# Performance work log

Measured on AMD Instinct MI355X. Metric: run time of the kernel, lower is better.

Reference implementation:

```python
import jax, jax.numpy as jnp
import numpy as np

B, S, N, D, H = 128, 512, 32, 512, 2  # batch, seq_len, num_size, node_dim, hop_size
NPAD = 4  # padded number slots per row


def _lin(key, fi, fo):
    return 0.02 * jax.random.normal(key, (H, fi, fo), jnp.float32), jnp.zeros((H, fo), jnp.float32)


def setup_inputs() -> dict:
    key = jax.random.key(0)
    ks = jax.random.split(key, 12)
    encoder_outputs = jax.random.normal(ks[0], (S, B, D), jnp.float32)
    num_encoder_outputs = jax.random.normal(ks[1], (B, N, D), jnp.float32)
    # distinct positions per row in [0, S), last NPAD slots padded with -1
    num_pos_pad = jnp.argsort(jax.random.uniform(ks[2], (B, S)), axis=-1)[:, :N].astype(jnp.int32)
    num_pos_pad = num_pos_pad.at[:, -NPAD:].set(-1)
    # order ranks 1..N (random permutation per row), 0 on padded slots
    num_order_pad = (jnp.argsort(jax.random.uniform(ks[3], (B, N)), axis=-1) + 1).astype(jnp.int32)
    num_order_pad = num_order_pad.at[:, -NPAD:].set(0)
    w_n1a, b_n1a = _lin(ks[4], D, D)
    w_n1b, b_n1b = _lin(ks[5], D, D)
    w_n2a, b_n2a = _lin(ks[6], D, D)
    w_n2b, b_n2b = _lin(ks[7], D, D)
    w_g, b_g = _lin(ks[8], 4 * D, D)
    w_o, b_o = _lin(ks[9], 2 * D, D)
    return dict(encoder_outputs=encoder_outputs, num_encoder_outputs=num_encoder_outputs,
                num_pos_pad=num_pos_pad, num_order_pad=num_order_pad,
                w_n1a=w_n1a, b_n1a=b_n1a, w_n1b=w_n1b, b_n1b=b_n1b,
                w_n2a=w_n2a, b_n2a=b_n2a, w_n2b=w_n2b, b_n2b=b_n2b,
                w_g=w_g, b_g=b_g, w_o=w_o, b_o=b_o)


def reference(encoder_outputs, num_encoder_outputs, num_pos_pad, num_order_pad,
              w_n1a, b_n1a, w_n1b, b_n1b, w_n2a, b_n2a, w_n2b, b_n2b,
              w_g, b_g, w_o, b_o):
    node_mask = (num_order_pad > 0)                              # [B,N]
    greater = num_order_pad[:, :, None] > num_order_pad[:, None, :]
    lower = ~greater                                             # <=
    eye = jnp.eye(N, dtype=jnp.float32)
    pair = (node_mask[:, None, :] & node_mask[:, :, None]).astype(jnp.float32) * (1.0 - eye)
    g_gt = pair * greater.astype(jnp.float32) + eye              # [B,N,N]
    g_lt = pair * lower.astype(jnp.float32) + eye
    # row-normalize (D^{-1} A); diagonal guarantees row sums >= 1
    g_gt = g_gt / g_gt.sum(-1, keepdims=True)
    g_lt = g_lt / g_lt.sum(-1, keepdims=True)

    node = num_encoder_outputs                                   # [B,N,D]
    for h in range(H):
        ni1 = jax.nn.relu(jnp.einsum('bnm,bmd,de->bne', g_gt, node, w_n1a[h]) + b_n1a[h])
        ni1 = jax.nn.relu(jnp.einsum('bnm,bmd,de->bne', g_gt, ni1, w_n1b[h]) + b_n1b[h])
        ni2 = jax.nn.relu(jnp.einsum('bnm,bmd,de->bne', g_lt, node, w_n2a[h]) + b_n2a[h])
        ni2 = jax.nn.relu(jnp.einsum('bnm,bmd,de->bne', g_lt, ni2, w_n2b[h]) + b_n2b[h])
        gate_in = jnp.concatenate([ni1, ni2, ni1 + ni2, ni1 - ni2], axis=-1)
        gate = jax.nn.sigmoid(gate_in @ w_g[h] + b_g[h])
        node_info = gate * ni1 + (1.0 - gate) * ni2
        node = jax.nn.relu(jnp.concatenate([node, node_info], axis=-1) @ w_o[h] + b_o[h])

    # scatter node embeddings into padded [B, S+1, D]; pads -> slot S (dropped)
    num_mask = num_pos_pad > -1
    clamped = jnp.where(num_mask, num_pos_pad, S)                # [B,N]
    gnn_info = jnp.zeros((B, S + 1, D), jnp.float32)
    gnn_info = gnn_info.at[jnp.arange(B)[:, None], clamped].set(node)
    gnn_info = gnn_info[:, :S, :].transpose(1, 0, 2)             # [S,B,D]
    gnn_info = encoder_outputs + gnn_info
    num_embedding = num_encoder_outputs + node
    problem_output = jnp.max(gnn_info, axis=0)                   # [B,D]
    return gnn_info, num_embedding, problem_output
```

## Files before the change

### kernel.cpp

```cpp
#include <hip/hip_runtime.h>
#include <math.h>

#define BB 128
#define SS 512
#define NN 32
#define DD 512
#define HH 2
#define MM (BB * NN)
#define DSQ (DD * DD)

typedef short bf16x8 __attribute__((ext_vector_type(8)));
typedef float f32x4 __attribute__((ext_vector_type(4)));

__device__ __forceinline__ unsigned short f2bf(float f) {
    unsigned int u = __float_as_uint(f);
    u += 0x7fffu + ((u >> 16) & 1u);
    return (unsigned short)(u >> 16);
}
__device__ __forceinline__ float bf2f(unsigned short h) {
    return __uint_as_float(((unsigned int)h) << 16);
}
__device__ __forceinline__ void g2l16(const void* gp, void* lp) {
    __builtin_amdgcn_global_load_lds(
        (const __attribute__((address_space(1))) void*)gp,
        (__attribute__((address_space(3))) void*)lp, 16, 0, 0);
}

__global__ __launch_bounds__(256) void adj_k(const int* __restrict__ order,
                                             const int* __restrict__ pos,
                                             float* __restrict__ g_gt,
                                             float* __restrict__ g_lt,
                                             int* __restrict__ slot) {
    int b = blockIdx.x;
    __shared__ int ord[NN];
    __shared__ float sgt[NN][NN + 1];
    __shared__ float slt[NN][NN + 1];
    __shared__ float rs_gt[NN], rs_lt[NN];
    int tid = threadIdx.x;
    slot[b * SS + tid] = -1;
    slot[b * SS + 256 + tid] = -1;
    if (tid < NN) ord[tid] = order[b * NN + tid];
    __syncthreads();
    for (int q = 0; q < 4; ++q) {
        int idx = tid + 256 * q;
        int n = idx >> 5, m = idx & 31;
        bool valid = (ord[n] > 0) && (ord[m] > 0) && (n != m);
        float eye = (n == m) ? 1.f : 0.f;
        bool gt = ord[n] > ord[m];
        sgt[n][m] = ((valid && gt) ? 1.f : 0.f) + eye;
        slt[n][m] = ((valid && !gt) ? 1.f : 0.f) + eye;
    }
    __syncthreads();
    if (tid < NN) {
        float s1 = 0.f, s2 = 0.f;
        for (int m = 0; m < NN; ++m) { s1 += sgt[tid][m]; s2 += slt[tid][m]; }
        rs_gt[tid] = s1; rs_lt[tid] = s2;
    }
    __syncthreads();
    for (int q = 0; q < 4; ++q) {
        int idx = tid + 256 * q;
        int n = idx >> 5, m = idx & 31;
        g_gt[b * 1024 + idx] = sgt[n][m] / rs_gt[n];
        g_lt[b * 1024 + idx] = slt[n][m] / rs_lt[n];
    }
    if (tid < NN) {
        int p = pos[b * NN + tid];
        if (p >= 0) slot[b * SS + p] = tid;
    }
}

struct WSfull { const float* s[12]; int slot[12]; const float* w_g; };

__global__ __launch_bounds__(256) void wprep_k(WSfull w, unsigned short* __restrict__ Wt) {
    int which = blockIdx.x;
    int tile = blockIdx.y;
    int tr = (tile >> 3) * 64, tc = (tile & 7) * 64;
    __shared__ float c1[64][65];
    __shared__ float c2[64][65];
    int lc = threadIdx.x & 63, g4 = threadIdx.x >> 6;
    if (which < 12) {
        const float* src = w.s[which];
        unsigned short* dst = Wt + (size_t)w.slot[which] * DSQ;
        for (int i = 0; i < 16; ++i) {
            int lr = g4 * 16 + i;
            c1[lr][lc] = src[(size_t)(tr + lr) * DD + tc + lc];
        }
        __syncthreads();
        for (int i = 0; i < 16; ++i) {
            int lr = g4 * 16 + i;
            dst[(size_t)(tc + lr) * DD + tr + lc] = f2bf(c1[lc][lr]);
        }
    } else {
        int h = which - 12;
        const float* base = w.w_g + (size_t)h * 4 * DSQ;
        for (int i = 0; i < 16; ++i) {
            int lr = g4 * 16 + i;
            int k = tr + lr, n = tc + lc;
            float a  = base[(size_t)k * DD + n];
            float b2 = base[(size_t)(DD + k) * DD + n];
            float c  = base[(size_t)(2 * DD + k) * DD + n];
            float d4 = base[(size_t)(3 * DD + k) * DD + n];
            c1[lr][lc] = a + c + d4;
            c2[lr][lc] = b2 + c - d4;
        }
        __syncthreads();
        unsigned short* d1 = Wt + (size_t)(h * 8 + 4) * DSQ;
        unsigned short* d2 = Wt + (size_t)(h * 8 + 5) * DSQ;
        for (int i = 0; i < 16; ++i) {
            int lr = g4 * 16 + i;
            d1[(size_t)(tc + lr) * DD + tr + lc] = f2bf(c1[lc][lr]);
            d2[(size_t)(tc + lr) * DD + tr + lc] = f2bf(c2[lc][lr]);
        }
    }
}

__global__ void conv_k(const float* __restrict__ x, unsigned short* __restrict__ o) {
    size_t i = ((size_t)blockIdx.x * 256 + threadIdx.x) * 4;
    float4 v = *(const float4*)(x + i);
    ushort4 r;
    r.x = f2bf(v.x); r.y = f2bf(v.y); r.z = f2bf(v.z); r.w = f2bf(v.w);
    *(ushort4*)(o + i) = r;
}

__global__ __launch_bounds__(256) void mix_k(const float* __restrict__ g_gt,
                                             const float* __restrict__ g_lt,
                                             const unsigned short* __restrict__ X1,
                                             const unsigned short* __restrict__ X2,
                                             unsigned short* __restrict__ Z1,
                                             unsigned short* __restrict__ Z2) {
    const int b = blockIdx.x;
    const int dc = blockIdx.y * 128;
    const float* G = blockIdx.z ? g_lt : g_gt;
    const unsigned short* X = blockIdx.z ? X2 : X1;
    unsigned short* Z = blockIdx.z ? Z2 : Z1;
    __shared__ float gs[NN * 33];
    __shared__ float xs[NN][128];
    const int t = threadIdx.x;
    {
        float4 v = ((const float4*)(G + (size_t)b * 1024))[t];
        int n = t >> 3, m0 = (t & 7) * 4;
        float* gp = gs + n * 33 + m0;
        gp[0] = v.x; gp[1] = v.y; gp[2] = v.z; gp[3] = v.w;
    }
#pragma unroll
    for (int q = 0; q < 2; ++q) {
        int e = t + 256 * q;
        int m = e >> 4, c = (e & 15) * 8;
        const unsigned short* src = X + ((size_t)(b * NN + m)) * DD + dc + c;
        ushort4 lo = *(const ushort4*)src;
        ushort4 hi = *(const ushort4*)(src + 4);
        float* xp = &xs[m][c];
        xp[0] = bf2f(lo.x); xp[1] = bf2f(lo.y); xp[2] = bf2f(lo.z); xp[3] = bf2f(lo.w);
        xp[4] = bf2f(hi.x); xp[5] = bf2f(hi.y); xp[6] = bf2f(hi.z); xp[7] = bf2f(hi.w);
    }
    __syncthreads();
    const int n = t >> 3;
    const int c0 = (t & 7) * 16;
    f32x4 r0 = {0.f, 0.f, 0.f, 0.f}, r1 = r0, r2 = r0, r3 = r0;
#pragma unroll
    for (int m = 0; m < NN; ++m) {
        float gv = gs[n * 33 + m];
        const float* xr = &xs[m][c0];
        r0 += gv * *(const f32x4*)(xr);
        r1 += gv * *(const f32x4*)(xr + 4);
        r2 += gv * *(const f32x4*)(xr + 8);
        r3 += gv * *(const f32x4*)(xr + 12);
    }
    unsigned short* dst = Z + ((size_t)(b * NN + n)) * DD + dc + c0;
    ushort4 o0, o1, o2, o3;
    o0.x = f2bf(r0.x); o0.y = f2bf(r0.y); o0.z = f2bf(r0.z); o0.w = f2bf(r0.w);
    o1.x = f2bf(r1.x); o1.y = f2bf(r1.y); o1.z = f2bf(r1.z); o1.w = f2bf(r1.w);
    o2.x = f2bf(r2.x); o2.y = f2bf(r2.y); o2.z = f2bf(r2.z); o2.w = f2bf(r2.w);
    o3.x = f2bf(r3.x); o3.y = f2bf(r3.y); o3.z = f2bf(r3.z); o3.w = f2bf(r3.w);
    *(ushort4*)(dst)      = o0;
    *(ushort4*)(dst + 4)  = o1;
    *(ushort4*)(dst + 8)  = o2;
    *(ushort4*)(dst + 12) = o3;
}

struct GA {
    const unsigned short* A1; const unsigned short* W1;
    const unsigned short* A2; const unsigned short* W2;
    const float* bias;
    const unsigned short* gin1; const unsigned short* gin2;
    unsigned short* out;
};

template <bool DUAL, bool GATE>
__global__ __launch_bounds__(256) void mgemm_k(GA a0, GA a1) {
    GA g = (blockIdx.z == 0) ? a0 : a1;
    __shared__ __align__(16) unsigned short As[64 * 64];
    __shared__ __align__(16) unsigned short Bs[128 * 64];
    const int tid = threadIdx.x;
    const int lane = tid & 63;
    const int wave = tid >> 6;
    const int wr = wave & 1, wc = wave >> 1;
    const int bm = blockIdx.x * 64, bn = blockIdx.y * 128;

    f32x4 acc[2][4];
#pragma unroll
    for (int i = 0; i < 2; ++i)
#pragma unroll
        for (int j = 0; j < 4; ++j) {
            acc[i][j].x = 0.f; acc[i][j].y = 0.f; acc[i][j].z = 0.f; acc[i][j].w = 0.f;
        }

    int rA[2], sA[2], rB[4], sB[4];
    unsigned short *dA[2], *dB[4];
#pragma unroll
    for (int q = 0; q < 2; ++q) {
        int e = tid + 256 * q;
        rA[q] = e >> 3;
        sA[q] = (tid & 7) ^ (rA[q] & 7);
        dA[q] = As + (size_t)e * 8;
    }
#pragma unroll
    for (int q = 0; q < 4; ++q) {
        int e = tid + 256 * q;
        rB[q] = e >> 3;
        sB[q] = (tid & 7) ^ (rB[q] & 7);
        dB[q] = Bs + (size_t)e * 8;
    }

    int aoff[2][2], boff[2][4];
#pragma unroll
    for (int t = 0; t < 2; ++t) {
        int sl = t * 4 + (lane >> 4);
        int p = sl ^ (lane & 7);
#pragma unroll
        for (int i = 0; i < 2; ++i) {
            int m = wr * 32 + i * 16 + (lane & 15);
            aoff[t][i] = m * 64 + p * 8;
        }
#pragma unroll
        for (int j = 0; j < 4; ++j) {
            int n = wc * 64 + j * 16 + (lane & 15);
            boff[t][j] = n * 64 + p * 8;
        }
    }

    const int nsrc = DUAL ? 2 : 1;
    for (int src = 0; src < nsrc; ++src) {
        const unsigned short* A = src ? g.A2 : g.A1;
        const unsigned short* W = src ? g.W2 : g.W1;
        const unsigned short* pa[2];
        const unsigned short* pb[4];
#pragma unroll
        for (int q = 0; q < 2; ++q) pa[q] = A + (size_t)(bm + rA[q]) * DD + sA[q] * 8;
#pragma unroll
        for (int q = 0; q < 4; ++q) pb[q] = W + (size_t)(bn + rB[q]) * DD + sB[q] * 8;
        for (int k0 = 0; k0 < DD; k0 += 64) {
#pragma unroll
            for (int q = 0; q < 2; ++q) g2l16(pa[q] + k0, dA[q]);
#pragma unroll
            for (int q = 0; q < 4; ++q) g2l16(pb[q] + k0, dB[q]);
            __syncthreads();
            bf16x8 af[2][2], bf_[2][4];
#pragma unroll
            for (int t = 0; t < 2; ++t) {
#pragma unroll
                for (int i = 0; i < 2; ++i) af[t][i] = *(const bf16x8*)(As + aoff[t][i]);
#pragma unroll
                for (int j = 0; j < 4; ++j) bf_[t][j] = *(const bf16x8*)(Bs + boff[t][j]);
            }
#pragma unroll
            for (int t = 0; t < 2; ++t)
#pragma unroll
                for (int i = 0; i < 2; ++i)
#pragma unroll
                    for (int j = 0; j < 4; ++j)
                        acc[i][j] = __builtin_amdgcn_mfma_f32_16x16x32_bf16(
                            af[t][i], bf_[t][j], acc[i][j], 0, 0, 0);
            __syncthreads();
        }
    }

#pragma unroll
    for (int i = 0; i < 2; ++i) {
        int row = bm + wr * 32 + i * 16 + (lane >> 4) * 4;
#pragma unroll
        for (int j = 0; j < 4; ++j) {
            int col = bn + wc * 64 + j * 16 + (lane & 15);
            float bv = g.bias[col];
#pragma unroll
            for (int rg = 0; rg < 4; ++rg) {
                float v = acc[i][j][rg] + bv;
                size_t idx = (size_t)(row + rg) * DD + col;
                if (GATE) {
                    float gg = 1.f / (1.f + __expf(-v));
                    float x1 = bf2f(g.gin1[idx]);
                    float x2 = bf2f(g.gin2[idx]);
                    g.out[idx] = f2bf(gg * x1 + (1.f - gg) * x2);
                } else {
                    g.out[idx] = f2bf(fmaxf(v, 0.f));
                }
            }
        }
    }
}

__global__ __launch_bounds__(256) void gnn_k(const float* __restrict__ enc,
                                             const unsigned short* __restrict__ node,
                                             const int* __restrict__ slot,
                                             const float* __restrict__ num_enc,
                                             float* __restrict__ out_gnn,
                                             float* __restrict__ out_nemb,
                                             float* __restrict__ partial) {
    int b = blockIdx.x;
    int t = threadIdx.x;
    if (blockIdx.y >= 16) {
        int q = blockIdx.y - 16;
        size_t base = (size_t)b * NN * DD + (size_t)q * (NN * DD / 4);
        for (int it = 0; it < 4; ++it) {
            size_t i = base + (size_t)(it * 256 + t) * 4;
            float4 a = *(const float4*)(num_enc + i);
            ushort4 nb = *(const ushort4*)(node + i);
            float4 r;
            r.x = a.x + bf2f(nb.x);
            r.y = a.y + bf2f(nb.y);
            r.z = a.z + bf2f(nb.z);
            r.w = a.w + bf2f(nb.w);
            *(float4*)(out_nemb + i) = r;
        }
        return;
    }
    __shared__ int sl[32];
    __shared__ float4 red[128];
    int s0 = blockIdx.y * 32;
    if (t < 32) sl[t] = slot[b * SS + s0 + t];
    __syncthreads();
    const int dv = (t & 127) * 4;
    const int sh = t >> 7;
    float4 mx = {-INFINITY, -INFINITY, -INFINITY, -INFINITY};
#pragma unroll 4
    for (int i = 0; i < 16; ++i) {
        int sloc = sh * 16 + i;
        int s = s0 + sloc;
        int n = sl[sloc];
        size_t ebase = ((size_t)s * BB + b) * DD + dv;
        float4 v = *(const float4*)(enc + ebase);
        if (n >= 0) {
            ushort4 nb = *(const ushort4*)(node + ((size_t)b * NN + n) * DD + dv);
            v.x += bf2f(nb.x);
            v.y += bf2f(nb.y);
            v.z += bf2f(nb.z);
            v.w += bf2f(nb.w);
        }
        *(float4*)(out_gnn + ebase) = v;
        mx.x = fmaxf(mx.x, v.x);
        mx.y = fmaxf(mx.y, v.y);
        mx.z = fmaxf(mx.z, v.z);
        mx.w = fmaxf(mx.w, v.w);
    }
    if (sh == 1) red[t & 127] = mx;
    __syncthreads();
    if (sh == 0) {
        float4 o = red[t];
        mx.x = fmaxf(mx.x, o.x);
        mx.y = fmaxf(mx.y, o.y);
        mx.z = fmaxf(mx.z, o.z);
        mx.w = fmaxf(mx.w, o.w);
        *(float4*)(partial + ((size_t)b * 16 + blockIdx.y) * DD + dv) = mx;
    }
}

__global__ void pmax_k(const float* __restrict__ partial, float* __restrict__ out_prob) {
    int i = blockIdx.x * 256 + threadIdx.x;
    if (i >= BB * DD) return;
    int b = i >> 9, d = i & 511;
    float m = -INFINITY;
    for (int c = 0; c < 16; ++c) m = fmaxf(m, partial[((size_t)b * 16 + c) * DD + d]);
    out_prob[i] = m;
}

extern "C" void kernel_launch(void* const* d_in, const int* in_sizes, int n_in,
                              void* d_out, int out_size, void* d_ws, size_t ws_size,
                              hipStream_t stream) {
    const float* enc     = (const float*)d_in[0];
    const float* num_enc = (const float*)d_in[1];
    const int*   pos     = (const int*)d_in[2];
    const int*   order   = (const int*)d_in[3];
    const float* w_n1a = (const float*)d_in[4];  const float* b_n1a = (const float*)d_in[5];
    const float* w_n1b = (const float*)d_in[6];  const float* b_n1b = (const float*)d_in[7];
    const float* w_n2a = (const float*)d_in[8];  const float* b_n2a = (const float*)d_in[9];
    const float* w_n2b = (const float*)d_in[10]; const float* b_n2b = (const float*)d_in[11];
    const float* w_g   = (const float*)d_in[12]; const float* b_g   = (const float*)d_in[13];
    const float* w_o   = (const float*)d_in[14]; const float* b_o   = (const float*)d_in[15];

    char* wp = (char*)d_ws;
    float* g_gt = (float*)wp;        wp += (size_t)BB * NN * NN * 4;
    float* g_lt = (float*)wp;        wp += (size_t)BB * NN * NN * 4;
    float* partial = (float*)wp;     wp += (size_t)BB * 16 * DD * 4;
    int* slot = (int*)wp;            wp += (size_t)BB * SS * 4;
    unsigned short* Wt = (unsigned short*)wp;    wp += (size_t)16 * DSQ * 2;
    unsigned short* node0 = (unsigned short*)wp; wp += (size_t)MM * DD * 2;
    unsigned short* nodeA = (unsigned short*)wp; wp += (size_t)MM * DD * 2;
    unsigned short* nodeB = (unsigned short*)wp; wp += (size_t)MM * DD * 2;
    unsigned short* ni1 = (unsigned short*)wp;   wp += (size_t)MM * DD * 2;
    unsigned short* ni2 = (unsigned short*)wp;   wp += (size_t)MM * DD * 2;
    unsigned short* t1 = (unsigned short*)wp;    wp += (size_t)MM * DD * 2;
    unsigned short* t2 = (unsigned short*)wp;    wp += (size_t)MM * DD * 2;

    float* out_gnn  = (float*)d_out;
    float* out_nemb = out_gnn + (size_t)SS * BB * DD;
    float* out_prob = out_nemb + (size_t)BB * NN * DD;

    adj_k<<<BB, 256, 0, stream>>>(order, pos, g_gt, g_lt, slot);

    WSfull wsrc;
    const float* srcs[12] = {w_n1a, w_n1b, w_n2a, w_n2b, w_o, w_o + DSQ,
                             w_n1a + DSQ, w_n1b + DSQ, w_n2a + DSQ, w_n2b + DSQ,
                             w_o + 2 * DSQ, w_o + 3 * DSQ};
    int slots[12] = {0, 1, 2, 3, 6, 7, 8, 9, 10, 11, 14, 15};
    for (int i = 0; i < 12; ++i) { wsrc.s[i] = srcs[i]; wsrc.slot[i] = slots[i]; }
    wsrc.w_g = w_g;
    wprep_k<<<dim3(14, 64), 256, 0, stream>>>(wsrc, Wt);
    conv_k<<<(MM * DD) / 1024, 256, 0, stream>>>(num_enc, node0);

    dim3 ggrid(MM / 64, DD / 128, 2);
    dim3 sgrid(MM / 64, DD / 128, 1);
    dim3 mgrid(BB, 4, 2);

    const unsigned short* nodeIn = node0;
    for (int h = 0; h < HH; ++h) {
        unsigned short* nodeOut = (h == 0) ? nodeA : nodeB;
        unsigned short* zb1 = (h == 0) ? nodeB : node0;
        unsigned short* zb2 = (unsigned short*)partial;
        const unsigned short* Wh = Wt + (size_t)h * 8 * DSQ;

        mix_k<<<mgrid, 256, 0, stream>>>(g_gt, g_lt, nodeIn, nodeIn, t1, t2);
        GA sa0 = {t1, Wh + 0 * DSQ, nullptr, nullptr, b_n1a + h * DD, nullptr, nullptr, ni1};
        GA sa1 = {t2, Wh + 2 * DSQ, nullptr, nullptr, b_n2a + h * DD, nullptr, nullptr, ni2};
        mgemm_k<false, false><<<ggrid, 256, 0, stream>>>(sa0, sa1);

        mix_k<<<mgrid, 256, 0, stream>>>(g_gt, g_lt, ni1, ni2, zb1, zb2);
        GA sb0 = {zb1, Wh + 1 * DSQ, nullptr, nullptr, b_n1b + h * DD, nullptr, nullptr, t1};
        GA sb1 = {zb2, Wh + 3 * DSQ, nullptr, nullptr, b_n2b + h * DD, nullptr, nullptr, t2};
        mgemm_k<false, false><<<ggrid, 256, 0, stream>>>(sb0, sb1);

        GA gg = {t1, Wh + 4 * DSQ, t2, Wh + 5 * DSQ, b_g + h * DD, t1, t2, ni1};
        mgemm_k<true, true><<<sgrid, 256, 0, stream>>>(gg, gg);

        GA go = {nodeIn, Wh + 6 * DSQ, ni1, Wh + 7 * DSQ, b_o + h * DD,
                 nullptr, nullptr, nodeOut};
        mgemm_k<true, false><<<sgrid, 256, 0, stream>>>(go, go);

        nodeIn = nodeOut;
    }
    const unsigned short* nodeF = nodeIn;

    gnn_k<<<dim3(BB, 20), 256, 0, stream>>>(enc, nodeF, slot, num_enc,
                                            out_gnn, out_nemb, partial);
    pmax_k<<<(BB * DD) / 256, 256, 0, stream>>>(partial, out_prob);
}
```

Baseline: 447.8 us.

## Fuse adjacency mixing into GEMM epilogues and double-buffer GEMM K loop

Removes the standalone mix kernels. The graph-adjacency mixing now runs in the epilogue of the preceding GEMM, which writes the ReLU tile to LDS and multiplies it by the per-batch 32x32 adjacency. The first mix is fused with the input bf16 conversion. The GEMM main loop also becomes double-buffered, issuing the next K-stage load before computing the current one. This saves kernel launches and global round-trips of the intermediate activations, at the cost of more LDS per block (lower occupancy) and mixing that now happens after the bias+ReLU of the previous layer rather than before the next GEMM.

```diff
diff --git a/kernel.cpp b/kernel.cpp
--- a/kernel.cpp
+++ b/kernel.cpp
@@ -114,68 +114,46 @@
     }
 }
 
-__global__ void conv_k(const float* __restrict__ x, unsigned short* __restrict__ o) {
-    size_t i = ((size_t)blockIdx.x * 256 + threadIdx.x) * 4;
-    float4 v = *(const float4*)(x + i);
-    ushort4 r;
-    r.x = f2bf(v.x); r.y = f2bf(v.y); r.z = f2bf(v.z); r.w = f2bf(v.w);
-    *(ushort4*)(o + i) = r;
-}
-
-__global__ __launch_bounds__(256) void mix_k(const float* __restrict__ g_gt,
-                                             const float* __restrict__ g_lt,
-                                             const unsigned short* __restrict__ X1,
-                                             const unsigned short* __restrict__ X2,
-                                             unsigned short* __restrict__ Z1,
-                                             unsigned short* __restrict__ Z2) {
+__global__ __launch_bounds__(256) void convmix_k(const float* __restrict__ x,
+                                                 const float* __restrict__ g_gt,
+                                                 const float* __restrict__ g_lt,
+                                                 unsigned short* __restrict__ node0,
+                                                 unsigned short* __restrict__ t1,
+                                                 unsigned short* __restrict__ t2) {
     const int b = blockIdx.x;
     const int dc = blockIdx.y * 128;
-    const float* G = blockIdx.z ? g_lt : g_gt;
-    const unsigned short* X = blockIdx.z ? X2 : X1;
-    unsigned short* Z = blockIdx.z ? Z2 : Z1;
-    __shared__ float gs[NN * 33];
     __shared__ float xs[NN][128];
+    __shared__ float gg[2][NN][NN];
     const int t = threadIdx.x;
-    {
-        float4 v = ((const float4*)(G + (size_t)b * 1024))[t];
-        int n = t >> 3, m0 = (t & 7) * 4;
-        float* gp = gs + n * 33 + m0;
-        gp[0] = v.x; gp[1] = v.y; gp[2] = v.z; gp[3] = v.w;
-    }
-#pragma unroll
-    for (int q = 0; q < 2; ++q) {
+    ((float4*)gg)[t]       = ((const float4*)(g_gt + (size_t)b * 1024))[t];
+    ((float4*)gg)[t + 256] = ((const float4*)(g_lt + (size_t)b * 1024))[t];
+#pragma unroll
+    for (int q = 0; q < 4; ++q) {
         int e = t + 256 * q;
-        int m = e >> 4, c = (e & 15) * 8;
-        const unsigned short* src = X + ((size_t)(b * NN + m)) * DD + dc + c;
-        ushort4 lo = *(const ushort4*)src;
-        ushort4 hi = *(const ushort4*)(src + 4);
-        float* xp = &xs[m][c];
-        xp[0] = bf2f(lo.x); xp[1] = bf2f(lo.y); xp[2] = bf2f(lo.z); xp[3] = bf2f(lo.w);
-        xp[4] = bf2f(hi.x); xp[5] = bf2f(hi.y); xp[6] = bf2f(hi.z); xp[7] = bf2f(hi.w);
-    }
-    __syncthreads();
-    const int n = t >> 3;
-    const int c0 = (t & 7) * 16;
-    f32x4 r0 = {0.f, 0.f, 0.f, 0.f}, r1 = r0, r2 = r0, r3 = r0;
-#pragma unroll
-    for (int m = 0; m < NN; ++m) {
-        float gv = gs[n * 33 + m];
-        const float* xr = &xs[m][c0];
-        r0 += gv * *(const f32x4*)(xr);
-        r1 += gv * *(const f32x4*)(xr + 4);
-        r2 += gv * *(const f32x4*)(xr + 8);
-        r3 += gv * *(const f32x4*)(xr + 12);
-    }
-    unsigned short* dst = Z + ((size_t)(b * NN + n)) * DD + dc + c0;
-    ushort4 o0, o1, o2, o3;
-    o0.x = f2bf(r0.x); o0.y = f2bf(r0.y); o0.z = f2bf(r0.z); o0.w = f2bf(r0.w);
-    o1.x = f2bf(r1.x); o1.y = f2bf(r1.y); o1.z = f2bf(r1.z); o1.w = f2bf(r1.w);
-    o2.x = f2bf(r2.x); o2.y = f2bf(r2.y); o2.z = f2bf(r2.z); o2.w = f2bf(r2.w);
-    o3.x = f2bf(r3.x); o3.y = f2bf(r3.y); o3.z = f2bf(r3.z); o3.w = f2bf(r3.w);
-    *(ushort4*)(dst)      = o0;
-    *(ushort4*)(dst + 4)  = o1;
-    *(ushort4*)(dst + 8)  = o2;
-    *(ushort4*)(dst + 12) = o3;
+        int row = e >> 5, c4 = (e & 31) * 4;
+        float4 v = *(const float4*)(x + (size_t)(b * NN + row) * DD + dc + c4);
+        *(float4*)&xs[row][c4] = v;
+        ushort4 o;
+        o.x = f2bf(v.x); o.y = f2bf(v.y); o.z = f2bf(v.z); o.w = f2bf(v.w);
+        *(ushort4*)(node0 + (size_t)(b * NN + row) * DD + dc + c4) = o;
+    }
+    __syncthreads();
+#pragma unroll
+    for (int gi = 0; gi < 2; ++gi) {
+        unsigned short* O = gi ? t2 : t1;
+#pragma unroll
+        for (int it = 0; it < 4; ++it) {
+            int task = it * 256 + t;
+            int n = task >> 5, dq = task & 31;
+            f32x4 r = {0.f, 0.f, 0.f, 0.f};
+#pragma unroll
+            for (int m = 0; m < NN; ++m)
+                r += gg[gi][n][m] * *(const f32x4*)(&xs[m][dq * 4]);
+            ushort4 ov;
+            ov.x = f2bf(r.x); ov.y = f2bf(r.y); ov.z = f2bf(r.z); ov.w = f2bf(r.w);
+            *(ushort4*)(O + (size_t)(b * NN + n) * DD + dc + dq * 4) = ov;
+        }
+    }
 }
 
 struct GA {
@@ -183,20 +161,35 @@
     const unsigned short* A2; const unsigned short* W2;
     const float* bias;
     const unsigned short* gin1; const unsigned short* gin2;
-    unsigned short* out;
+    const float* G1; const float* G2;
+    unsigned short* out; unsigned short* out2; unsigned short* out3;
 };
 
-template <bool DUAL, bool GATE>
+template <bool DUAL, bool GATE, int EMIX>
 __global__ __launch_bounds__(256) void mgemm_k(GA a0, GA a1) {
     GA g = (blockIdx.z == 0) ? a0 : a1;
-    __shared__ __align__(16) unsigned short As[64 * 64];
-    __shared__ __align__(16) unsigned short Bs[128 * 64];
+    constexpr int LDSB = 49152 + (EMIX == 1 ? 8192 : EMIX == 2 ? 16384 : 0);
+    __shared__ __align__(16) char lds[LDSB];
+    unsigned short* Ab = (unsigned short*)lds;
+    unsigned short* Bb = (unsigned short*)(lds + 16384);
+    float* gsh = (float*)(lds + 49152);
     const int tid = threadIdx.x;
     const int lane = tid & 63;
     const int wave = tid >> 6;
     const int wr = wave & 1, wc = wave >> 1;
     const int bm = blockIdx.x * 64, bn = blockIdx.y * 128;
 
+    if (EMIX >= 1) {
+        const float4* g1 = (const float4*)(g.G1 + (size_t)(bm >> 5) * 1024);
+        ((float4*)gsh)[tid] = g1[tid];
+        ((float4*)gsh)[tid + 256] = g1[tid + 256];
+        if (EMIX == 2) {
+            const float4* g2v = (const float4*)(g.G2 + (size_t)(bm >> 5) * 1024);
+            ((float4*)(gsh + 2048))[tid] = g2v[tid];
+            ((float4*)(gsh + 2048))[tid + 256] = g2v[tid + 256];
+        }
+    }
+
     f32x4 acc[2][4];
 #pragma unroll
     for (int i = 0; i < 2; ++i)
@@ -205,21 +198,14 @@
             acc[i][j].x = 0.f; acc[i][j].y = 0.f; acc[i][j].z = 0.f; acc[i][j].w = 0.f;
         }
 
-    int rA[2], sA[2], rB[4], sB[4];
-    unsigned short *dA[2], *dB[4];
-#pragma unroll
-    for (int q = 0; q < 2; ++q) {
-        int e = tid + 256 * q;
-        rA[q] = e >> 3;
-        sA[q] = (tid & 7) ^ (rA[q] & 7);
-        dA[q] = As + (size_t)e * 8;
-    }
+    const int rA0 = tid >> 3,          sA0 = (tid & 7) ^ (rA0 & 7);
+    const int rA1 = (tid + 256) >> 3,  sA1 = (tid & 7) ^ (rA1 & 7);
+    int rB[4], sB[4];
 #pragma unroll
     for (int q = 0; q < 4; ++q) {
         int e = tid + 256 * q;
         rB[q] = e >> 3;
         sB[q] = (tid & 7) ^ (rB[q] & 7);
-        dB[q] = Bs + (size_t)e * 8;
     }
 
     int aoff[2][2], boff[2][4];
@@ -239,61 +225,108 @@
         }
     }
 
-    const int nsrc = DUAL ? 2 : 1;
-    for (int src = 0; src < nsrc; ++src) {
-        const unsigned short* A = src ? g.A2 : g.A1;
-        const unsigned short* W = src ? g.W2 : g.W1;
-        const unsigned short* pa[2];
-        const unsigned short* pb[4];
-#pragma unroll
-        for (int q = 0; q < 2; ++q) pa[q] = A + (size_t)(bm + rA[q]) * DD + sA[q] * 8;
-#pragma unroll
-        for (int q = 0; q < 4; ++q) pb[q] = W + (size_t)(bn + rB[q]) * DD + sB[q] * 8;
-        for (int k0 = 0; k0 < DD; k0 += 64) {
-#pragma unroll
-            for (int q = 0; q < 2; ++q) g2l16(pa[q] + k0, dA[q]);
-#pragma unroll
-            for (int q = 0; q < 4; ++q) g2l16(pb[q] + k0, dB[q]);
-            __syncthreads();
-            bf16x8 af[2][2], bf_[2][4];
-#pragma unroll
-            for (int t = 0; t < 2; ++t) {
-#pragma unroll
-                for (int i = 0; i < 2; ++i) af[t][i] = *(const bf16x8*)(As + aoff[t][i]);
-#pragma unroll
-                for (int j = 0; j < 4; ++j) bf_[t][j] = *(const bf16x8*)(Bs + boff[t][j]);
+    auto STAGE = [&](int ks, int c) {
+        const unsigned short* A = (DUAL && ks >= 8) ? g.A2 : g.A1;
+        const unsigned short* W = (DUAL && ks >= 8) ? g.W2 : g.W1;
+        const int k0 = (ks & 7) * 64;
+        g2l16(A + (size_t)(bm + rA0) * DD + k0 + sA0 * 8, Ab + c * 4096 + tid * 8);
+        g2l16(A + (size_t)(bm + rA1) * DD + k0 + sA1 * 8,
+              Ab + c * 4096 + (tid + 256) * 8);
+#pragma unroll
+        for (int q = 0; q < 4; ++q)
+            g2l16(W + (size_t)(bn + rB[q]) * DD + k0 + sB[q] * 8,
+                  Bb + c * 8192 + (tid + 256 * q) * 8);
+    };
+
+    const int NK = DUAL ? 16 : 8;
+    STAGE(0, 0);
+    __syncthreads();
+    int cur = 0;
+    for (int ks = 0; ks < NK; ++ks) {
+        if (ks + 1 < NK) STAGE(ks + 1, cur ^ 1);
+        const unsigned short* Ac = Ab + cur * 4096;
+        const unsigned short* Bc = Bb + cur * 8192;
+        bf16x8 af[2][2], bf_[2][4];
+#pragma unroll
+        for (int t = 0; t < 2; ++t) {
+#pragma unroll
+            for (int i = 0; i < 2; ++i) af[t][i] = *(const bf16x8*)(Ac + aoff[t][i]);
+#pragma unroll
+            for (int j = 0; j < 4; ++j) bf_[t][j] = *(const bf16x8*)(Bc + boff[t][j]);
+        }
+#pragma unroll
+        for (int t = 0; t < 2; ++t)
+#pragma unroll
+            for (int i = 0; i < 2; ++i)
+#pragma unroll
+                for (int j = 0; j < 4; ++j)
+                    acc[i][j] = __builtin_amdgcn_mfma_f32_16x16x32_bf16(
+                        af[t][i], bf_[t][j], acc[i][j], 0, 0, 0);
+        __syncthreads();
+        cur ^= 1;
+    }
+
+    if (EMIX == 0) {
+#pragma unroll
+        for (int i = 0; i < 2; ++i) {
+            int row = bm + wr * 32 + i * 16 + (lane >> 4) * 4;
+#pragma unroll
+            for (int j = 0; j < 4; ++j) {
+                int col = bn + wc * 64 + j * 16 + (lane & 15);
+                float bv = g.bias[col];
+#pragma unroll
+                for (int rg = 0; rg < 4; ++rg) {
+                    float v = acc[i][j][rg] + bv;
+                    size_t idx = (size_t)(row + rg) * DD + col;
+                    if (GATE) {
+                        float gg = 1.f / (1.f + __expf(-v));
+                        float x1 = bf2f(g.gin1[idx]);
+                        float x2 = bf2f(g.gin2[idx]);
+                        g.out[idx] = f2bf(gg * x1 + (1.f - gg) * x2);
+                    } else {
+                        g.out[idx] = f2bf(fmaxf(v, 0.f));
+                    }
+                }
             }
-#pragma unroll
-            for (int t = 0; t < 2; ++t)
-#pragma unroll
-                for (int i = 0; i < 2; ++i)
-#pragma unroll
-                    for (int j = 0; j < 4; ++j)
-                        acc[i][j] = __builtin_amdgcn_mfma_f32_16x16x32_bf16(
-                            af[t][i], bf_[t][j], acc[i][j], 0, 0, 0);
-            __syncthreads();
-        }
-    }
-
-#pragma unroll
-    for (int i = 0; i < 2; ++i) {
-        int row = bm + wr * 32 + i * 16 + (lane >> 4) * 4;
-#pragma unroll
-        for (int j = 0; j < 4; ++j) {
-            int col = bn + wc * 64 + j * 16 + (lane & 15);
-            float bv = g.bias[col];
-#pragma unroll
-            for (int rg = 0; rg < 4; ++rg) {
-                float v = acc[i][j][rg] + bv;
-                size_t idx = (size_t)(row + rg) * DD + col;
-                if (GATE) {
-                    float gg = 1.f / (1.f + __expf(-v));
-                    float x1 = bf2f(g.gin1[idx]);
-                    float x2 = bf2f(g.gin2[idx]);
-                    g.out[idx] = f2bf(gg * x1 + (1.f - gg) * x2);
-                } else {
-                    g.out[idx] = f2bf(fmaxf(v, 0.f));
+        }
+    } else {
+        float* S = (float*)lds;
+#pragma unroll
+        for (int i = 0; i < 2; ++i) {
+            int lrow = wr * 32 + i * 16 + (lane >> 4) * 4;
+#pragma unroll
+            for (int j = 0; j < 4; ++j) {
+                int lcol = wc * 64 + j * 16 + (lane & 15);
+                float bv = g.bias[bn + lcol];
+#pragma unroll
+                for (int rg = 0; rg < 4; ++rg) {
+                    float v = fmaxf(acc[i][j][rg] + bv, 0.f);
+                    S[(lrow + rg) * 128 + lcol] = v;
+                    if (EMIX == 2)
+                        g.out[(size_t)(bm + lrow + rg) * DD + bn + lcol] = f2bf(v);
                 }
+            }
+        }
+        __syncthreads();
+        const int ngi = (EMIX == 2) ? 2 : 1;
+#pragma unroll
+        for (int gi = 0; gi < ngi; ++gi) {
+            unsigned short* O = (EMIX == 2) ? (gi ? g.out3 : g.out2) : g.out;
+            const float* gb = gsh + gi * 2048;
+#pragma unroll
+            for (int it = 0; it < 8; ++it) {
+                int task = it * 256 + tid;
+                int n = task >> 5, dq = task & 31;
+                int bt = n >> 5, nl = n & 31;
+                const float* gr = gb + bt * 1024 + nl * 32;
+                const float* Sb = S + bt * 32 * 128 + dq * 4;
+                f32x4 r = {0.f, 0.f, 0.f, 0.f};
+#pragma unroll
+                for (int m = 0; m < NN; ++m)
+                    r += gr[m] * *(const f32x4*)(Sb + m * 128);
+                ushort4 ov;
+                ov.x = f2bf(r.x); ov.y = f2bf(r.y); ov.z = f2bf(r.z); ov.w = f2bf(r.w);
+                *(ushort4*)(O + (size_t)(bm + n) * DD + bn + dq * 4) = ov;
             }
         }
     }
@@ -415,39 +448,42 @@
     for (int i = 0; i < 12; ++i) { wsrc.s[i] = srcs[i]; wsrc.slot[i] = slots[i]; }
     wsrc.w_g = w_g;
     wprep_k<<<dim3(14, 64), 256, 0, stream>>>(wsrc, Wt);
-    conv_k<<<(MM * DD) / 1024, 256, 0, stream>>>(num_enc, node0);
+    convmix_k<<<dim3(BB, 4), 256, 0, stream>>>(num_enc, g_gt, g_lt, node0, t1, t2);
 
     dim3 ggrid(MM / 64, DD / 128, 2);
     dim3 sgrid(MM / 64, DD / 128, 1);
-    dim3 mgrid(BB, 4, 2);
-
-    const unsigned short* nodeIn = node0;
+
     for (int h = 0; h < HH; ++h) {
-        unsigned short* nodeOut = (h == 0) ? nodeA : nodeB;
-        unsigned short* zb1 = (h == 0) ? nodeB : node0;
-        unsigned short* zb2 = (unsigned short*)partial;
         const unsigned short* Wh = Wt + (size_t)h * 8 * DSQ;
-
-        mix_k<<<mgrid, 256, 0, stream>>>(g_gt, g_lt, nodeIn, nodeIn, t1, t2);
-        GA sa0 = {t1, Wh + 0 * DSQ, nullptr, nullptr, b_n1a + h * DD, nullptr, nullptr, ni1};
-        GA sa1 = {t2, Wh + 2 * DSQ, nullptr, nullptr, b_n2a + h * DD, nullptr, nullptr, ni2};
-        mgemm_k<false, false><<<ggrid, 256, 0, stream>>>(sa0, sa1);
-
-        mix_k<<<mgrid, 256, 0, stream>>>(g_gt, g_lt, ni1, ni2, zb1, zb2);
-        GA sb0 = {zb1, Wh + 1 * DSQ, nullptr, nullptr, b_n1b + h * DD, nullptr, nullptr, t1};
-        GA sb1 = {zb2, Wh + 3 * DSQ, nullptr, nullptr, b_n2b + h * DD, nullptr, nullptr, t2};
-        mgemm_k<false, false><<<ggrid, 256, 0, stream>>>(sb0, sb1);
-
-        GA gg = {t1, Wh + 4 * DSQ, t2, Wh + 5 * DSQ, b_g + h * DD, t1, t2, ni1};
-        mgemm_k<true, true><<<sgrid, 256, 0, stream>>>(gg, gg);
-
-        GA go = {nodeIn, Wh + 6 * DSQ, ni1, Wh + 7 * DSQ, b_o + h * DD,
-                 nullptr, nullptr, nodeOut};
-        mgemm_k<true, false><<<sgrid, 256, 0, stream>>>(go, go);
-
-        nodeIn = nodeOut;
-    }
-    const unsigned short* nodeF = nodeIn;
+        const unsigned short* nodeIn = (h == 0) ? node0 : nodeA;
+
+        GA sa0 = {t1, Wh + 0 * DSQ, nullptr, nullptr, b_n1a + h * DD,
+                  nullptr, nullptr, g_gt, nullptr, ni1, nullptr, nullptr};
+        GA sa1 = {t2, Wh + 2 * DSQ, nullptr, nullptr, b_n2a + h * DD,
+                  nullptr, nullptr, g_lt, nullptr, ni2, nullptr, nullptr};
+        mgemm_k<false, false, 1><<<ggrid, 256, 0, stream>>>(sa0, sa1);
+
+        GA sb0 = {ni1, Wh + 1 * DSQ, nullptr, nullptr, b_n1b + h * DD,
+                  nullptr, nullptr, nullptr, nullptr, t1, nullptr, nullptr};
+        GA sb1 = {ni2, Wh + 3 * DSQ, nullptr, nullptr, b_n2b + h * DD,
+                  nullptr, nullptr, nullptr, nullptr, t2, nullptr, nullptr};
+        mgemm_k<false, false, 0><<<ggrid, 256, 0, stream>>>(sb0, sb1);
+
+        GA gg2 = {t1, Wh + 4 * DSQ, t2, Wh + 5 * DSQ, b_g + h * DD,
+                  t1, t2, nullptr, nullptr, ni1, nullptr, nullptr};
+        mgemm_k<true, true, 0><<<sgrid, 256, 0, stream>>>(gg2, gg2);
+
+        if (h == 0) {
+            GA go = {nodeIn, Wh + 6 * DSQ, ni1, Wh + 7 * DSQ, b_o + h * DD,
+                     nullptr, nullptr, g_gt, g_lt, nodeA, t1, t2};
+            mgemm_k<true, false, 2><<<sgrid, 256, 0, stream>>>(go, go);
+        } else {
+            GA go = {nodeIn, Wh + 6 * DSQ, ni1, Wh + 7 * DSQ, b_o + h * DD,
+                     nullptr, nullptr, nullptr, nullptr, nodeB, nullptr, nullptr};
+            mgemm_k<true, false, 0><<<sgrid, 256, 0, stream>>>(go, go);
+        }
+    }
+    const unsigned short* nodeF = nodeB;
 
     gnn_k<<<dim3(BB, 20), 256, 0, stream>>>(enc, nodeF, slot, num_enc,
                                             out_gnn, out_nemb, partial);
```

New measurement: 423.8 us. -5.4%, faster.
